# Optimization experiments

Hardware: AMD Instinct MI355X
Metric: run time of the kernel (lower is better)

Reference implementation:

```python
import jax, jax.numpy as jnp
import numpy as np
from jax import lax
from math import sqrt

POLE = sqrt(3.0) - 2.0                       # cubic B-spline pole
GAIN = (1.0 - POLE) * (1.0 - 1.0 / POLE)     # = 6.0
UPSAMPLING_FACTOR = 2


def _cubic_spline_1d(t):
    a = jnp.abs(t)
    out = (2.0 / 3.0 + (0.5 * a - 1.0) * a ** 2) * (a < 1)
    out = out + (-(a - 2.0) ** 3 / 6.0) * ((a >= 1) & (a < 2))
    return out


def _bspline_kernel(f):
    is_odd = f % 2
    k = 4 * f - is_odd
    start = (1 + is_odd) / (2 * f) - 2.0
    pts = jnp.arange(k, dtype=jnp.float32) * (1.0 / f) + start
    return _cubic_spline_1d(pts)


def _prefilter_1d(x, axis):
    """Causal + anticausal recursive cubic-spline coefficient filter along `axis`."""
    n = x.shape[axis]
    if n == 1:
        return x
    p = POLE
    xm = jnp.moveaxis(x * GAIN, axis, 0)  # (n, ...)
    i = np.arange(n)
    pows = jnp.asarray(p ** i + p ** (2 * n - 1 - i), dtype=x.dtype)
    # causal boundary condition (mirror)
    c0 = jnp.tensordot(pows, xm, axes=(0, 0)) * (p / (1.0 - p ** (2 * n))) + xm[0]

    def causal(carry, xi):
        y = xi + p * carry
        return y, y

    _, ys = lax.scan(causal, c0, xm[1:])
    cm = jnp.concatenate([c0[None], ys], axis=0)
    # anticausal boundary condition
    last = cm[-1] * (p / (p - 1.0))

    def anti(carry, ci):
        y = p * (carry - ci)
        return y, y

    _, ys2 = lax.scan(anti, last, cm[:-1], reverse=True)
    out = jnp.concatenate([ys2, last[None]], axis=0)
    return jnp.moveaxis(out, 0, axis)


def _upsample_1d(x, axis, kernel, f):
    """Strided transposed conv along `axis` with replicate padding of 2 (per-channel)."""
    dim_size = x.shape[axis]
    xm = jnp.moveaxis(x, axis, -1)
    lead = xm.shape[:-1]
    x3 = xm.reshape(-1, 1, dim_size)
    x3 = jnp.pad(x3, ((0, 0), (0, 0), (2, 2)), mode='edge')
    k = kernel.shape[0]
    implicit_padding = 7 * f // 2
    pad = k - 1 - implicit_padding  # conv_transpose == lhs-dilated correlation w/ flipped kernel
    out = lax.conv_general_dilated(
        x3,
        kernel[::-1][None, None, :],
        window_strides=(1,),
        padding=[(pad, pad)],
        lhs_dilation=(f,),
        dimension_numbers=('NCH', 'OIH', 'NCH'),
    )
    out = out.reshape(lead + (out.shape[-1],))
    return jnp.moveaxis(out, -1, axis)


def setup_inputs() -> dict:
    key = jax.random.key(0)
    volume = jax.random.normal(key, (2, 3, 96, 96, 96), dtype=jnp.float32)
    return {"volume": volume}


def reference(volume):
    f = UPSAMPLING_FACTOR
    kernel = _bspline_kernel(f).astype(volume.dtype)
    first_spatial_dim = min(volume.ndim - 1, 2)
    x = volume
    for axis in range(first_spatial_dim, volume.ndim):
        x = _prefilter_1d(x, axis)
    for axis in range(first_spatial_dim, volume.ndim):
        x = _upsample_1d(x, axis, kernel, f)
    return x
```

## Files before the change

### kernel.cpp

```cpp
#include <hip/hip_runtime.h>


#define TAPS 28
#define CHUNK 12
#define WIN (CHUNK + TAPS - 1)

__device__ double g_Wd[96 * 96];
__device__ float g_Mb[192 * TAPS];
__device__ float g_bufA[6 * 96 * 96 * 192];
__device__ float g_bufB[6 * 96 * 192 * 192];

__device__ __forceinline__ int clamp96(int j) { return j < 0 ? 0 : (j > 95 ? 95 : j); }

__global__ void compute_Wd_kernel(double* __restrict__ Wd) {
    int j = threadIdx.x;
    if (j >= 96) return;
    const double p = -0.26794919243112270647253365849413;
    double c[96];
    double pj = 1.0;
    for (int t = 0; t < j; ++t) pj *= p;
    double p191j = 1.0;
    for (int t = 0; t < 191 - j; ++t) p191j *= p;
    double p2n = 1.0;
    for (int t = 0; t < 192; ++t) p2n *= p;
    double K = p / (1.0 - p2n);
    double cur = 6.0 * K * (pj + p191j) + (j == 0 ? 6.0 : 0.0);
    c[0] = cur;
    for (int i = 1; i < 96; ++i) {
        cur = (i == j ? 6.0 : 0.0) + p * cur;
        c[i] = cur;
    }
    double nxt = cur * (p / (p - 1.0));
    Wd[95 * 96 + j] = nxt;
    for (int i = 94; i >= 0; --i) {
        nxt = p * (nxt - c[i]);
        Wd[i * 96 + j] = nxt;
    }
}

__global__ void compute_M_kernel(const double* __restrict__ Wd, float* __restrict__ Mb) {
    int i = threadIdx.x;
    if (i >= 192) return;
    const double cw[8] = {1.0 / 384.0, 121.0 / 384.0, 235.0 / 384.0, 27.0 / 384.0,
                          27.0 / 384.0, 235.0 / 384.0, 121.0 / 384.0, 1.0 / 384.0};
    int ph = i & 1;
    int c = i >> 1;
    for (int t = 0; t < TAPS; ++t) {
        int j = c - 13 + t;
        double m = 0.0;
        if (j >= 0 && j < 96) {
            for (int tt = 0; tt < 4; ++tt) {
                int k = c + ph - 2 + tt;
                k = k < 0 ? 0 : (k > 95 ? 95 : k);
                m += cw[ph * 4 + tt] * Wd[k * 96 + j];
            }
        }
        Mb[i * TAPS + t] = (float)m;
    }
}

__global__ __launch_bounds__(512) void pass_z(const float* __restrict__ in,
                                              float* __restrict__ out,
                                              const float* __restrict__ Mb) {
    __shared__ float s_in[64 * 97];
    __shared__ float s_out[64 * 193];
    float w0[TAPS], w1[TAPS];
#pragma unroll
    for (int t = 0; t < TAPS; ++t) {
        w0[t] = Mb[96 * TAPS + t];
        w1[t] = Mb[97 * TAPS + t];
    }
    size_t base = (size_t)blockIdx.x * 64;
    const float* src = in + base * 96;
    int tid = threadIdx.x;
    for (int k = tid; k < 64 * 96; k += 512)
        s_in[(k / 96) * 97 + (k % 96)] = src[k];
    __syncthreads();

    int lane = tid & 63;
    int wave = tid >> 6;
    int c0 = wave * CHUNK;
    const float* xl = s_in + lane * 97;
    float* op = s_out + lane * 193 + 2 * c0;
    float win[WIN];
#pragma unroll
    for (int k = 0; k < WIN; ++k) win[k] = xl[clamp96(c0 - 13 + k)];

    if (c0 >= 12 && c0 + CHUNK <= 84) {
#pragma unroll
        for (int mi = 0; mi < CHUNK; ++mi) {
            float a0 = 0.f, a1 = 0.f;
#pragma unroll
            for (int t = 0; t < TAPS; ++t) {
                float xv = win[mi + t];
                a0 = fmaf(w0[t], xv, a0);
                a1 = fmaf(w1[t], xv, a1);
            }
            op[2 * mi] = a0;
            op[2 * mi + 1] = a1;
        }
    } else {
#pragma unroll
        for (int mi = 0; mi < CHUNK; ++mi) {
            int m = c0 + mi;
            int wb = __builtin_amdgcn_readfirstlane(m * 2 * TAPS);
            const float* wr = Mb + wb;
            float a0 = 0.f, a1 = 0.f;
#pragma unroll
            for (int t = 0; t < TAPS; ++t) {
                float xv = win[mi + t];
                a0 = fmaf(wr[t], xv, a0);
                a1 = fmaf(wr[TAPS + t], xv, a1);
            }
            op[2 * mi] = a0;
            op[2 * mi + 1] = a1;
        }
    }
    __syncthreads();
    float* dst = out + base * 192;
    for (int k = tid; k < 64 * 192; k += 512)
        dst[k] = s_out[(k / 192) * 193 + (k % 192)];
}

template <int INNER, int SEG>
__global__ __launch_bounds__(256) void pass_line(const float* __restrict__ in,
                                                 float* __restrict__ out,
                                                 const float* __restrict__ Mb) {
    constexpr int SPAN = 96 / SEG;
    constexpr int CHUNKS = SPAN / CHUNK;
    float w0[TAPS], w1[TAPS];
#pragma unroll
    for (int t = 0; t < TAPS; ++t) {
        w0[t] = Mb[96 * TAPS + t];
        w1[t] = Mb[97 * TAPS + t];
    }
    int idx = blockIdx.x * 256 + threadIdx.x;
    int r = idx % INNER;
    int q = idx / INNER;
    int s = q % SEG;
    int o = q / SEG;
    const float* src = in + (size_t)o * 96 * INNER + r;
    float* dst = out + (size_t)o * 192 * INNER + r;
    int m0 = s * SPAN;
    float win[WIN];
#pragma unroll
    for (int k = 0; k < WIN; ++k) win[k] = src[(size_t)clamp96(m0 - 13 + k) * INNER];
    for (int ch = 0; ch < CHUNKS; ++ch) {
        int mc = m0 + ch * CHUNK;
        float* d = dst + (size_t)(2 * mc) * INNER;
        if (mc >= 12 && mc + CHUNK <= 84) {
#pragma unroll
            for (int mi = 0; mi < CHUNK; ++mi) {
                float a0 = 0.f, a1 = 0.f;
#pragma unroll
                for (int t = 0; t < TAPS; ++t) {
                    float xv = win[mi + t];
                    a0 = fmaf(w0[t], xv, a0);
                    a1 = fmaf(w1[t], xv, a1);
                }
                d[0] = a0;
                d[(size_t)INNER] = a1;
                d += (size_t)2 * INNER;
            }
        } else {
#pragma unroll
            for (int mi = 0; mi < CHUNK; ++mi) {
                int m = mc + mi;
                int wb = __builtin_amdgcn_readfirstlane(m * 2 * TAPS);
                const float* wr = Mb + wb;
                float a0 = 0.f, a1 = 0.f;
#pragma unroll
                for (int t = 0; t < TAPS; ++t) {
                    float xv = win[mi + t];
                    a0 = fmaf(wr[t], xv, a0);
                    a1 = fmaf(wr[TAPS + t], xv, a1);
                }
                d[0] = a0;
                d[(size_t)INNER] = a1;
                d += (size_t)2 * INNER;
            }
        }
        if (ch < CHUNKS - 1) {
#pragma unroll
            for (int k = 0; k < WIN - CHUNK; ++k) win[k] = win[k + CHUNK];
#pragma unroll
            for (int k = 0; k < CHUNK; ++k)
                win[WIN - CHUNK + k] = src[(size_t)clamp96(mc + (WIN - 13) + k) * INNER];
        }
    }
}

extern "C" void kernel_launch(void* const* d_in, const int* in_sizes, int n_in,
                              void* d_out, int out_size, void* d_ws, size_t ws_size,
                              hipStream_t stream) {
    const float* x = (const float*)d_in[0];
    float* out = (float*)d_out;
    double* Wd;
    float *Mb, *bufA, *bufB;
    hipGetSymbolAddress((void**)&Wd, HIP_SYMBOL(g_Wd));
    hipGetSymbolAddress((void**)&Mb, HIP_SYMBOL(g_Mb));
    hipGetSymbolAddress((void**)&bufA, HIP_SYMBOL(g_bufA));
    hipGetSymbolAddress((void**)&bufB, HIP_SYMBOL(g_bufB));

    compute_Wd_kernel<<<1, 96, 0, stream>>>(Wd);
    compute_M_kernel<<<1, 192, 0, stream>>>(Wd, Mb);

    pass_z<<<864, 512, 0, stream>>>(x, bufA, Mb);
    pass_line<192, 4><<<1728, 256, 0, stream>>>(bufA, bufB, Mb);
    pass_line<36864, 2><<<1728, 256, 0, stream>>>(bufB, out, Mb);
}
```

Baseline: 325.7 us.

## Replace sliding-window line passes with per-output float4 gather kernel

The y and x upsampling passes are rewritten so that each thread computes one coarse position's two output phases for four adjacent inner elements using float4 loads. All 28 taps are gathered directly instead of sliding a per-thread register window across chunks of the line. The full position-dependent weight matrix is staged in shared memory, which removes the interior/boundary branch split and the scalar weight reloads. This greatly increases thread-level parallelism and vectorizes memory access, at the cost of reading each input row many times and relying on L1/L2 reuse within a block.

```diff
diff --git a/kernel.cpp b/kernel.cpp
--- a/kernel.cpp
+++ b/kernel.cpp
@@ -122,72 +122,55 @@
         dst[k] = s_out[(k / 192) * 193 + (k % 192)];
 }
 
-template <int INNER, int SEG>
-__global__ __launch_bounds__(256) void pass_line(const float* __restrict__ in,
-                                                 float* __restrict__ out,
-                                                 const float* __restrict__ Mb) {
-    constexpr int SPAN = 96 / SEG;
-    constexpr int CHUNKS = SPAN / CHUNK;
-    float w0[TAPS], w1[TAPS];
+template <int INNER>
+__global__ __launch_bounds__(384) void pass_gather(const float* __restrict__ in,
+                                                   float* __restrict__ out,
+                                                   const float* __restrict__ Mb) {
+    constexpr int TILES = INNER / 32;
+    constexpr int IV = INNER / 4;
+    __shared__ float s_w[192 * TAPS];
+    int tid = threadIdx.x;
+    {
+        const float4* mb4 = (const float4*)Mb;
+        float4* sw4 = (float4*)s_w;
+        for (int k = tid; k < 192 * TAPS / 4; k += 384) sw4[k] = mb4[k];
+    }
+    __syncthreads();
+
+    int cb = blockIdx.x & 1;
+    int bi = blockIdx.x >> 1;
+    int rt = bi % TILES;
+    int o = bi / TILES;
+    int c = cb * 48 + (tid >> 3);
+    int r4 = rt * 8 + (tid & 7);
+
+    const float4* src = (const float4*)(in + (size_t)o * 96 * INNER) + r4;
+    float4* dst = (float4*)(out + (size_t)o * 192 * INNER) + r4;
+
+    float4 xv[TAPS];
+#pragma unroll
+    for (int t = 0; t < TAPS; ++t)
+        xv[t] = src[(size_t)clamp96(c - 13 + t) * IV];
+
+    const float* w0 = s_w + 2 * c * TAPS;
+    float4 a0 = make_float4(0.f, 0.f, 0.f, 0.f);
+    float4 a1 = make_float4(0.f, 0.f, 0.f, 0.f);
 #pragma unroll
     for (int t = 0; t < TAPS; ++t) {
-        w0[t] = Mb[96 * TAPS + t];
-        w1[t] = Mb[97 * TAPS + t];
+        float4 x = xv[t];
+        float b0 = w0[t];
+        float b1 = w0[TAPS + t];
+        a0.x = fmaf(b0, x.x, a0.x);
+        a0.y = fmaf(b0, x.y, a0.y);
+        a0.z = fmaf(b0, x.z, a0.z);
+        a0.w = fmaf(b0, x.w, a0.w);
+        a1.x = fmaf(b1, x.x, a1.x);
+        a1.y = fmaf(b1, x.y, a1.y);
+        a1.z = fmaf(b1, x.z, a1.z);
+        a1.w = fmaf(b1, x.w, a1.w);
     }
-    int idx = blockIdx.x * 256 + threadIdx.x;
-    int r = idx % INNER;
-    int q = idx / INNER;
-    int s = q % SEG;
-    int o = q / SEG;
-    const float* src = in + (size_t)o * 96 * INNER + r;
-    float* dst = out + (size_t)o * 192 * INNER + r;
-    int m0 = s * SPAN;
-    float win[WIN];
-#pragma unroll
-    for (int k = 0; k < WIN; ++k) win[k] = src[(size_t)clamp96(m0 - 13 + k) * INNER];
-    for (int ch = 0; ch < CHUNKS; ++ch) {
-        int mc = m0 + ch * CHUNK;
-        float* d = dst + (size_t)(2 * mc) * INNER;
-        if (mc >= 12 && mc + CHUNK <= 84) {
-#pragma unroll
-            for (int mi = 0; mi < CHUNK; ++mi) {
-                float a0 = 0.f, a1 = 0.f;
-#pragma unroll
-                for (int t = 0; t < TAPS; ++t) {
-                    float xv = win[mi + t];
-                    a0 = fmaf(w0[t], xv, a0);
-                    a1 = fmaf(w1[t], xv, a1);
-                }
-                d[0] = a0;
-                d[(size_t)INNER] = a1;
-                d += (size_t)2 * INNER;
-            }
-        } else {
-#pragma unroll
-            for (int mi = 0; mi < CHUNK; ++mi) {
-                int m = mc + mi;
-                int wb = __builtin_amdgcn_readfirstlane(m * 2 * TAPS);
-                const float* wr = Mb + wb;
-                float a0 = 0.f, a1 = 0.f;
-#pragma unroll
-                for (int t = 0; t < TAPS; ++t) {
-                    float xv = win[mi + t];
-                    a0 = fmaf(wr[t], xv, a0);
-                    a1 = fmaf(wr[TAPS + t], xv, a1);
-                }
-                d[0] = a0;
-                d[(size_t)INNER] = a1;
-                d += (size_t)2 * INNER;
-            }
-        }
-        if (ch < CHUNKS - 1) {
-#pragma unroll
-            for (int k = 0; k < WIN - CHUNK; ++k) win[k] = win[k + CHUNK];
-#pragma unroll
-            for (int k = 0; k < CHUNK; ++k)
-                win[WIN - CHUNK + k] = src[(size_t)clamp96(mc + (WIN - 13) + k) * INNER];
-        }
-    }
+    dst[(size_t)(2 * c) * IV] = a0;
+    dst[(size_t)(2 * c + 1) * IV] = a1;
 }
 
 extern "C" void kernel_launch(void* const* d_in, const int* in_sizes, int n_in,
@@ -206,6 +189,6 @@
     compute_M_kernel<<<1, 192, 0, stream>>>(Wd, Mb);
 
     pass_z<<<864, 512, 0, stream>>>(x, bufA, Mb);
-    pass_line<192, 4><<<1728, 256, 0, stream>>>(bufA, bufB, Mb);
-    pass_line<36864, 2><<<1728, 256, 0, stream>>>(bufB, out, Mb);
+    pass_gather<192><<<576 * 6 * 2, 384, 0, stream>>>(bufA, bufB, Mb);
+    pass_gather<36864><<<6 * 1152 * 2, 384, 0, stream>>>(bufB, out, Mb);
 }
```

Result: slower. 392.9 us (+20.6%).

## Stage y/x upsample lines through shared memory with vectorized tile loads

Applied to the files above, without the earlier changes.

Replaces the per-thread strided global-load line kernel with a block kernel that loads a 96x64 tile into shared memory using float4 loads. Each thread then reads its window from LDS and produces 24 outputs per line segment, split into 4 quarters along the line. The goal is to remove redundant overlapping global window reads and uncoalesced scalar loads across segments. The cost is a larger per-thread window of 51 registers, which may lower occupancy, and a shared-memory staging step with a barrier.

```diff
diff --git a/kernel.cpp b/kernel.cpp
--- a/kernel.cpp
+++ b/kernel.cpp
@@ -122,70 +122,71 @@
         dst[k] = s_out[(k / 192) * 193 + (k % 192)];
 }
 
-template <int INNER, int SEG>
-__global__ __launch_bounds__(256) void pass_line(const float* __restrict__ in,
-                                                 float* __restrict__ out,
-                                                 const float* __restrict__ Mb) {
-    constexpr int SPAN = 96 / SEG;
-    constexpr int CHUNKS = SPAN / CHUNK;
-    float w0[TAPS], w1[TAPS];
-#pragma unroll
-    for (int t = 0; t < TAPS; ++t) {
-        w0[t] = Mb[96 * TAPS + t];
-        w1[t] = Mb[97 * TAPS + t];
-    }
-    int idx = blockIdx.x * 256 + threadIdx.x;
-    int r = idx % INNER;
-    int q = idx / INNER;
-    int s = q % SEG;
-    int o = q / SEG;
-    const float* src = in + (size_t)o * 96 * INNER + r;
-    float* dst = out + (size_t)o * 192 * INNER + r;
-    int m0 = s * SPAN;
-    float win[WIN];
-#pragma unroll
-    for (int k = 0; k < WIN; ++k) win[k] = src[(size_t)clamp96(m0 - 13 + k) * INNER];
-    for (int ch = 0; ch < CHUNKS; ++ch) {
-        int mc = m0 + ch * CHUNK;
-        float* d = dst + (size_t)(2 * mc) * INNER;
-        if (mc >= 12 && mc + CHUNK <= 84) {
-#pragma unroll
-            for (int mi = 0; mi < CHUNK; ++mi) {
-                float a0 = 0.f, a1 = 0.f;
-#pragma unroll
-                for (int t = 0; t < TAPS; ++t) {
-                    float xv = win[mi + t];
-                    a0 = fmaf(w0[t], xv, a0);
-                    a1 = fmaf(w1[t], xv, a1);
-                }
-                d[0] = a0;
-                d[(size_t)INNER] = a1;
-                d += (size_t)2 * INNER;
-            }
-        } else {
-#pragma unroll
-            for (int mi = 0; mi < CHUNK; ++mi) {
-                int m = mc + mi;
-                int wb = __builtin_amdgcn_readfirstlane(m * 2 * TAPS);
-                const float* wr = Mb + wb;
-                float a0 = 0.f, a1 = 0.f;
-#pragma unroll
-                for (int t = 0; t < TAPS; ++t) {
-                    float xv = win[mi + t];
-                    a0 = fmaf(wr[t], xv, a0);
-                    a1 = fmaf(wr[TAPS + t], xv, a1);
-                }
-                d[0] = a0;
-                d[(size_t)INNER] = a1;
-                d += (size_t)2 * INNER;
-            }
-        }
-        if (ch < CHUNKS - 1) {
-#pragma unroll
-            for (int k = 0; k < WIN - CHUNK; ++k) win[k] = win[k + CHUNK];
-#pragma unroll
-            for (int k = 0; k < CHUNK; ++k)
-                win[WIN - CHUNK + k] = src[(size_t)clamp96(mc + (WIN - 13) + k) * INNER];
+template <int INNER>
+__global__ __launch_bounds__(256) void pass_staged(const float* __restrict__ in,
+                                                   float* __restrict__ out,
+                                                   const float* __restrict__ Mb) {
+    constexpr int CT = INNER / 64;
+    __shared__ float s[96 * 64];
+    int tid = threadIdx.x;
+    int ct = blockIdx.x % CT;
+    int o = blockIdx.x / CT;
+    const float* src = in + (size_t)o * 96 * INNER + (size_t)ct * 64;
+    float* dst = out + (size_t)o * 192 * INNER + (size_t)ct * 64;
+
+#pragma unroll
+    for (int it = 0; it < 6; ++it) {
+        int k = tid + it * 256;
+        int row = k >> 4;
+        int c4 = k & 15;
+        float4 v = *(const float4*)(src + (size_t)row * INNER + c4 * 4);
+        *(float4*)(&s[row * 64 + c4 * 4]) = v;
+    }
+    __syncthreads();
+
+    int col = tid & 63;
+    int cq = tid >> 6;
+    int c0 = cq * 24;
+
+    float win[51];
+#pragma unroll
+    for (int k = 0; k < 51; ++k) win[k] = s[clamp96(c0 - 13 + k) * 64 + col];
+
+    if (cq == 1 || cq == 2) {
+        float w0[TAPS], w1[TAPS];
+#pragma unroll
+        for (int t = 0; t < TAPS; ++t) {
+            w0[t] = Mb[96 * TAPS + t];
+            w1[t] = Mb[97 * TAPS + t];
+        }
+#pragma unroll
+        for (int mi = 0; mi < 24; ++mi) {
+            float a0 = 0.f, a1 = 0.f;
+#pragma unroll
+            for (int t = 0; t < TAPS; ++t) {
+                float xv = win[mi + t];
+                a0 = fmaf(w0[t], xv, a0);
+                a1 = fmaf(w1[t], xv, a1);
+            }
+            int m = c0 + mi;
+            dst[(size_t)(2 * m) * INNER + col] = a0;
+            dst[(size_t)(2 * m + 1) * INNER + col] = a1;
+        }
+    } else {
+#pragma unroll
+        for (int mi = 0; mi < 24; ++mi) {
+            int m = c0 + mi;
+            int wb = __builtin_amdgcn_readfirstlane(m * 2 * TAPS);
+            const float* wr = Mb + wb;
+            float a0 = 0.f, a1 = 0.f;
+#pragma unroll
+            for (int t = 0; t < TAPS; ++t) {
+                float xv = win[mi + t];
+                a0 = fmaf(wr[t], xv, a0);
+                a1 = fmaf(wr[TAPS + t], xv, a1);
+            }
+            dst[(size_t)(2 * m) * INNER + col] = a0;
+            dst[(size_t)(2 * m + 1) * INNER + col] = a1;
         }
     }
 }
@@ -206,6 +207,6 @@
     compute_M_kernel<<<1, 192, 0, stream>>>(Wd, Mb);
 
     pass_z<<<864, 512, 0, stream>>>(x, bufA, Mb);
-    pass_line<192, 4><<<1728, 256, 0, stream>>>(bufA, bufB, Mb);
-    pass_line<36864, 2><<<1728, 256, 0, stream>>>(bufB, out, Mb);
-}
+    pass_staged<192><<<1728, 256, 0, stream>>>(bufA, bufB, Mb);
+    pass_staged<36864><<<3456, 256, 0, stream>>>(bufB, out, Mb);
+}
```

Measured after the change: 332.0 us. About the same (+1.9%).
